# Optimization experiments

Hardware: AMD Instinct MI355X
Metric: run time of the kernel (lower is better)

## Reference

```python
import jax, jax.numpy as jnp
import numpy as np
import math

B, N_TOK, C, H = 8, 1024, 384, 6
K, S, P = 3, 2, 1
OUT_C, HID = 384, 4 * 384
EPS = 1e-5
NEG_INF = float('-inf')


def _build_conv_mask(num_token, k, s, p):
    """Replicates ConvAttentionMask (include_cls_token=True). Returns (mask[(N+2),(N+2)], idx[(W,k^2)] with -1 for padding)."""
    I = int(math.sqrt(num_token))
    ref = np.arange(num_token).reshape(I, I)
    ref = np.pad(ref, ((0, p), (0, p)), constant_values=-1)
    cent = np.arange(k // 2 - p, I - k // 2 + p, s)
    cc = np.stack(np.meshgrid(cent, cent, indexing='ij'), -1).reshape(-1, 1, 2)  # cartesian_prod order
    ke = np.arange(-(k // 2), k // 2 + 1)
    kc = np.stack(np.meshgrid(ke, ke, indexing='ij'), -1).reshape(1, -1, 2)
    coords = cc + kc  # (W, k^2, 2); negative coords wrap like torch fancy indexing -> hit -1 padding
    idx = ref[coords[..., 0], coords[..., 1]]  # (W, k^2)
    mask = np.full((num_token, num_token), NEG_INF, np.float32)
    for w in idx:
        v = w[w >= 0]
        mask[np.ix_(v, v)] = 1.0
    idx = idx + (idx >= 0).astype(np.int32)  # shift for cls token; -1 stays -1
    mask = np.pad(mask, ((1, 0), (1, 0)), constant_values=1.0)  # cls row/col
    mask = np.pad(mask, ((0, 1), (0, 1)), constant_values=0.0)  # extra zero-padded token
    return mask, idx

MASK_NP, IDX_NP = _build_conv_mask(N_TOK, K, S, P)
W_WIN = IDX_NP.shape[0]
# torch negative index -1 on a length-(N_TOK+1) tensor -> wrap to last token
IDX_FLAT = np.where(IDX_NP < 0, IDX_NP + N_TOK + 1, IDX_NP).reshape(-1)


def _ln(x, w, b):
    mu = jnp.mean(x, -1, keepdims=True)
    var = jnp.mean(jnp.square(x - mu), -1, keepdims=True)
    return (x - mu) * jax.lax.rsqrt(var + EPS) * w + b


def setup_inputs() -> dict:
    key = jax.random.key(0)
    ks = jax.random.split(key, 8)
    sd = 0.02
    return {
        'x': jax.random.normal(ks[0], (B, N_TOK + 1, C), jnp.float32),
        'norm1_w': jnp.ones((C,), jnp.float32), 'norm1_b': jnp.zeros((C,), jnp.float32),
        'qkv_w': sd * jax.random.normal(ks[1], (3 * C, C), jnp.float32),
        'proj_w': sd * jax.random.normal(ks[2], (C, C), jnp.float32),
        'proj_b': jnp.zeros((C,), jnp.float32),
        'norm2_w': jnp.ones((C,), jnp.float32), 'norm2_b': jnp.zeros((C,), jnp.float32),
        'pool_w': sd * jax.random.normal(ks[3], (C, K * K * C), jnp.float32),
        'pool_b': jnp.zeros((C,), jnp.float32),
        'norm3_w': jnp.ones((C,), jnp.float32), 'norm3_b': jnp.zeros((C,), jnp.float32),
        'fc1_w': sd * jax.random.normal(ks[4], (HID, C), jnp.float32),
        'fc1_b': jnp.zeros((HID,), jnp.float32),
        'fc2_w': sd * jax.random.normal(ks[5], (OUT_C, HID), jnp.float32),
        'fc2_b': jnp.zeros((OUT_C,), jnp.float32),
    }


def reference(x, norm1_w, norm1_b, qkv_w, proj_w, proj_b, norm2_w, norm2_b,
              pool_w, pool_b, norm3_w, norm3_b, fc1_w, fc1_b, fc2_w, fc2_b):
    mask = jnp.asarray(MASK_NP)  # (N_TOK+2, N_TOK+2), values in {-inf, 0, 1}
    Bv, N, Cv = x.shape
    d = Cv // H
    h = _ln(x, norm1_w, norm1_b)
    h = jnp.pad(h, ((0, 0), (0, 1), (0, 0)))  # append zero token -> (B, N+1, C)
    M = N + 1
    # attention (scale = num_heads**-0.5 as in the source, qkv has no bias)
    qkv = (h @ qkv_w.T).reshape(Bv, M, 3, H, d).transpose(2, 0, 3, 1, 4)
    q, k, v = qkv[0], qkv[1], qkv[2]
    scores = jnp.einsum('bhqd,bhkd->bhqk', q, k) * (H ** -0.5)
    # multiplicative mask {-inf,0,1}: keep where 1, zero where 0, -inf where -inf (intended semantics)
    scores = jnp.where(mask == 1.0, scores, jnp.where(mask == 0.0, 0.0, NEG_INF))
    probs = jax.nn.softmax(scores, axis=-1)
    attn = jnp.einsum('bhqk,bhkd->bhqd', probs, v).transpose(0, 2, 1, 3).reshape(Bv, M, Cv)
    attn = attn @ proj_w.T + proj_b
    h = h + attn
    h = h[:, :-1, :]  # drop padded token -> (B, N, C)
    h = _ln(h, norm2_w, norm2_b)
    # conv-style pooling: gather k^2 tokens per window, project
    gathered = h[:, IDX_FLAT, :].reshape(Bv, W_WIN, K * K * Cv)
    tok = gathered @ pool_w.T + pool_b  # (B, W, C)
    h = jnp.concatenate([h[:, :1, :], tok], axis=1)  # prepend cls -> (B, W+1, C)
    h = _ln(h, norm3_w, norm3_b)
    h = jax.nn.gelu(h @ fc1_w.T + fc1_b, approximate=False)
    return h @ fc2_w.T + fc2_b  # (B, W+1, OUT_C)
```

## Files before the change

kernel.cpp:

```cpp
#include <hip/hip_runtime.h>


typedef unsigned short u16;
typedef unsigned int u32;
typedef short s16x8 __attribute__((ext_vector_type(8)));
typedef float f32x4 __attribute__((ext_vector_type(4)));

__device__ __forceinline__ float b2f(u16 u) {
    return __uint_as_float(((u32)u) << 16);
}
__device__ __forceinline__ u16 f2b(float f) {
    u32 u = __float_as_uint(f);
    return (u16)((u + 0x7FFFu + ((u >> 16) & 1u)) >> 16);
}
__device__ __forceinline__ void gload16(const void* g, void* l) {
    __builtin_amdgcn_global_load_lds(
        (const __attribute__((address_space(1))) void*)g,
        (__attribute__((address_space(3))) void*)l, 16, 0, 0);
}
__device__ __forceinline__ float wave_sum(float v) {
#pragma unroll
    for (int o = 32; o > 0; o >>= 1) v += __shfl_xor(v, o, 64);
    return v;
}
__device__ __forceinline__ float wave_max(float v) {
#pragma unroll
    for (int o = 32; o > 0; o >>= 1) v = fmaxf(v, __shfl_xor(v, o, 64));
    return v;
}
__device__ __forceinline__ float half_sum(float v) {
#pragma unroll
    for (int o = 16; o > 0; o >>= 1) v += __shfl_xor(v, o, 64);
    return v;
}
__device__ __forceinline__ float half_max(float v) {
#pragma unroll
    for (int o = 16; o > 0; o >>= 1) v = fmaxf(v, __shfl_xor(v, o, 64));
    return v;
}
__device__ __forceinline__ float dot8(const float* qsh, int d0, uint4 u) {
    return qsh[d0 + 0] * b2f((u16)(u.x)) + qsh[d0 + 1] * b2f((u16)(u.x >> 16)) +
           qsh[d0 + 2] * b2f((u16)(u.y)) + qsh[d0 + 3] * b2f((u16)(u.y >> 16)) +
           qsh[d0 + 4] * b2f((u16)(u.z)) + qsh[d0 + 5] * b2f((u16)(u.z >> 16)) +
           qsh[d0 + 6] * b2f((u16)(u.w)) + qsh[d0 + 7] * b2f((u16)(u.w >> 16));
}

#define CCH 384
#define SCALE 0.40824829046386302f
#define NEG_BIG (-1e30f)

#define W_QKV 0
#define W_PROJ 442368
#define W_POOL 589824
#define W_FC1 1916928
#define W_FC2 2506752
#define W_TOTAL 3096576

__device__ __forceinline__ void ln_from_f32(const float* in, const float* w,
                                            const float* bb, u16* out,
                                            int lane) {
    float v[6];
    float s = 0.f, ss = 0.f;
#pragma unroll
    for (int i = 0; i < 6; i++) {
        v[i] = in[lane + 64 * i];
        s += v[i];
        ss += v[i] * v[i];
    }
    s = wave_sum(s);
    ss = wave_sum(ss);
    float mu = s * (1.f / 384.f);
    float var = ss * (1.f / 384.f) - mu * mu;
    float inv = rsqrtf(var + 1e-5f);
#pragma unroll
    for (int i = 0; i < 6; i++) {
        int c = lane + 64 * i;
        out[c] = f2b((v[i] - mu) * inv * w[c] + bb[c]);
    }
}
__device__ __forceinline__ void ln_from_b16(const u16* in, const float* w,
                                            const float* bb, u16* out,
                                            int lane) {
    float v[6];
    float s = 0.f, ss = 0.f;
#pragma unroll
    for (int i = 0; i < 6; i++) {
        v[i] = b2f(in[lane + 64 * i]);
        s += v[i];
        ss += v[i] * v[i];
    }
    s = wave_sum(s);
    ss = wave_sum(ss);
    float mu = s * (1.f / 384.f);
    float var = ss * (1.f / 384.f) - mu * mu;
    float inv = rsqrtf(var + 1e-5f);
#pragma unroll
    for (int i = 0; i < 6; i++) {
        int c = lane + 64 * i;
        out[c] = f2b((v[i] - mu) * inv * w[c] + bb[c]);
    }
}

#define PRO_LN 2052
#define PRO_CVT 1512
#define PRO_ZERO 771
__global__ __launch_bounds__(256) void prologue(
    const float* __restrict__ x, const float* __restrict__ n1w,
    const float* __restrict__ n1b, u16* __restrict__ h1,
    const float* __restrict__ qkv_w, const float* __restrict__ proj_w,
    const float* __restrict__ pool_w, const float* __restrict__ fc1_w,
    const float* __restrict__ fc2_w, u16* __restrict__ wb,
    float* __restrict__ dout) {
    int bid = blockIdx.x, tid = threadIdx.x;
    if (bid < PRO_LN) {
        int wv = tid >> 6, lane = tid & 63;
        int row = bid * 4 + wv;
        int t = row % 1026, b = row / 1026;
        u16* out = h1 + (size_t)row * CCH;
        if (t == 1025) {
#pragma unroll
            for (int i = 0; i < 6; i++) out[lane + 64 * i] = 0;
            return;
        }
        ln_from_f32(x + ((size_t)b * 1025 + t) * CCH, n1w, n1b, out, lane);
    } else if (bid < PRO_LN + PRO_CVT) {
        size_t off = ((size_t)(bid - PRO_LN) * 256 + tid) * 8;
        if (off >= W_TOTAL) return;
        const float* src;
        size_t base;
        if (off < W_PROJ)       { src = qkv_w;  base = W_QKV; }
        else if (off < W_POOL)  { src = proj_w; base = W_PROJ; }
        else if (off < W_FC1)   { src = pool_w; base = W_POOL; }
        else if (off < W_FC2)   { src = fc1_w;  base = W_FC1; }
        else                    { src = fc2_w;  base = W_FC2; }
        size_t rel = off - base;
        float4 a = *(const float4*)(src + rel);
        float4 b = *(const float4*)(src + rel + 4);
        uint4 o;
        o.x = (u32)f2b(a.x) | ((u32)f2b(a.y) << 16);
        o.y = (u32)f2b(a.z) | ((u32)f2b(a.w) << 16);
        o.z = (u32)f2b(b.x) | ((u32)f2b(b.y) << 16);
        o.w = (u32)f2b(b.z) | ((u32)f2b(b.w) << 16);
        *(uint4*)(wb + off) = o;
    } else {
        size_t idx = ((size_t)(bid - PRO_LN - PRO_CVT) * 256 + tid) * 4;
        *(float4*)(dout + idx) = make_float4(0.f, 0.f, 0.f, 0.f);
    }
}

#define MID_LN 2050
#define MID_ZERO 768
__global__ __launch_bounds__(256) void midk(u16* __restrict__ h,
                                            const float* __restrict__ n2w,
                                            const float* __restrict__ n2b,
                                            float* __restrict__ tokf) {
    int bid = blockIdx.x, tid = threadIdx.x;
    if (bid < MID_LN) {
        int wv = tid >> 6, lane = tid & 63;
        int row = bid * 4 + wv;
        int b = row / 1025, t = row % 1025;
        u16* p = h + ((size_t)b * 1026 + t) * CCH;
        ln_from_b16(p, n2w, n2b, p, lane);
    } else {
        size_t idx = ((size_t)(bid - MID_LN) * 256 + tid) * 4;
        *(float4*)(tokf + idx) = make_float4(0.f, 0.f, 0.f, 0.f);
    }
}

__global__ __launch_bounds__(256) void ln3_concat(const u16* __restrict__ h2,
                                                  const float* __restrict__ tokf,
                                                  const float* __restrict__ w,
                                                  const float* __restrict__ bb,
                                                  u16* __restrict__ h3) {
    int tid = threadIdx.x;
    int wv = tid >> 6, lane = tid & 63;
    int row = blockIdx.x * 4 + wv;
    int b = row / 257, t = row % 257;
    u16* out = h3 + (size_t)row * CCH;
    if (t == 0) {
        ln_from_b16(h2 + (size_t)b * 1026 * CCH, w, bb, out, lane);
    } else {
        ln_from_f32(tokf + ((size_t)b * 256 + (t - 1)) * CCH, w, bb, out, lane);
    }
}

template <int TN, bool GATHER, int SPLITK, bool BIAS, bool GELU_ACT, bool RES,
          bool ATOMIC>
__global__ __launch_bounds__(256) void gemm_mf(const u16* __restrict__ A,
                                               int lda,
                                               const u16* __restrict__ Bwb,
                                               const float* __restrict__ bias,
                                               const u16* __restrict__ Res,
                                               void* __restrict__ Yv, int M,
                                               int N, int K) {
    __shared__ u16 Asl[128 * 32];
    __shared__ u16 Bsl[TN * 32];
    const int tid = threadIdx.x;
    const int wave = tid >> 6, lane = tid & 63;
    const int quad = lane >> 4, l15 = lane & 15;
    const int wvu = __builtin_amdgcn_readfirstlane(wave);
    const int m0 = blockIdx.y * 128, n0 = blockIdx.x * TN;
    const int kp = (SPLITK > 1) ? blockIdx.z : 0;
    const int KS = K / SPLITK;
    const int kbase = kp * KS;
    const int srow = tid >> 2;
    const int sseg = (tid & 3) ^ (srow & 3);

    f32x4 acc[2][TN / 16];
#pragma unroll
    for (int i = 0; i < 2; i++)
#pragma unroll
        for (int j = 0; j < TN / 16; j++) acc[i][j] = (f32x4){0.f, 0.f, 0.f, 0.f};

    for (int kt = 0; kt < KS; kt += 32) {
        const int kk = kbase + kt;
        const int kf = kk + sseg * 8;
#pragma unroll
        for (int L = 0; L < 2; L++) {
            int row = L * 64 + srow;
            const u16* src;
            if (GATHER) {
                int m = m0 + row;
                int b = m >> 8, w = m & 255;
                int j = kf / 384, rem = kf - j * 384;
                int pr = 2 * (w >> 4) + j / 3 - 1;
                int pc = 2 * (w & 15) + j % 3 - 1;
                int tok = (pr >= 0 && pr < 32 && pc >= 0 && pc < 32)
                              ? (32 * pr + pc + 1)
                              : 1024;
                src = A + ((size_t)b * 1026 + tok) * 384 + rem;
            } else {
                int m = m0 + row;
                if (m >= M) m = M - 1;
                src = A + (size_t)m * lda + kf;
            }
            gload16(src, &Asl[(size_t)(L * 256 + wvu * 64) * 8]);
        }
#pragma unroll
        for (int L = 0; L < TN / 64; L++) {
            int row = L * 64 + srow;
            gload16(Bwb + (size_t)(n0 + row) * K + kf,
                    &Bsl[(size_t)(L * 256 + wvu * 64) * 8]);
        }
        __syncthreads();
        s16x8 afr[2], bfr[TN / 16];
        const int rslot = (quad ^ (l15 & 3)) * 8;
#pragma unroll
        for (int ms = 0; ms < 2; ms++)
            afr[ms] =
                *(const s16x8*)(&Asl[(wave * 32 + ms * 16 + l15) * 32 + rslot]);
#pragma unroll
        for (int ns = 0; ns < TN / 16; ns++)
            bfr[ns] = *(const s16x8*)(&Bsl[(ns * 16 + l15) * 32 + rslot]);
#pragma unroll
        for (int ms = 0; ms < 2; ms++)
#pragma unroll
            for (int ns = 0; ns < TN / 16; ns++)
                acc[ms][ns] = __builtin_amdgcn_mfma_f32_16x16x32_bf16(
                    afr[ms], bfr[ns], acc[ms][ns], 0, 0, 0);
        __syncthreads();
    }
#pragma unroll
    for (int ms = 0; ms < 2; ms++) {
#pragma unroll
        for (int ns = 0; ns < TN / 16; ns++) {
            int n = n0 + ns * 16 + l15;
#pragma unroll
            for (int i = 0; i < 4; i++) {
                int m = m0 + wave * 32 + ms * 16 + quad * 4 + i;
                if (m >= M) continue;
                float v = acc[ms][ns][i];
                if (BIAS && (SPLITK == 1 || kp == 0)) v += bias[n];
                if (RES) v += b2f(Res[(size_t)m * N + n]);
                if (GELU_ACT) v = 0.5f * v * (1.f + erff(v * 0.70710678118f));
                if (ATOMIC)
                    atomicAdd((float*)Yv + (size_t)m * N + n, v);
                else
                    ((u16*)Yv)[(size_t)m * N + n] = f2b(v);
            }
        }
    }
}

__global__ __launch_bounds__(1024) void attn_win(u16* __restrict__ qkv) {
    int bid = blockIdx.x;
    int tid = threadIdx.x;
    if (bid < 48) {
        int h = bid % 6, b = bid / 6;
        u16* base = qkv + (size_t)b * 1026 * 1152 + h * 64;
        int lane = tid & 63, wv = tid >> 6;
        __shared__ float sc[1026];
        __shared__ float qsh[64];
        __shared__ float redmax[16], redsum[16];
        __shared__ float pv[16][64];
        if (tid < 64) qsh[tid] = b2f(base[tid]);
        __syncthreads();
        for (int key = tid; key < 1026; key += 1024) {
            const u16* krow = base + (size_t)key * 1152 + 384;
            float acc = 0.f;
#pragma unroll
            for (int d0 = 0; d0 < 64; d0 += 8)
                acc += dot8(qsh, d0, *(const uint4*)(krow + d0));
            sc[key] = acc * SCALE;
        }
        __syncthreads();
        float lm = NEG_BIG;
        for (int key = tid; key < 1026; key += 1024) lm = fmaxf(lm, sc[key]);
        lm = wave_max(lm);
        if (lane == 0) redmax[wv] = lm;
        __syncthreads();
        float mx = NEG_BIG;
#pragma unroll
        for (int i = 0; i < 16; i++) mx = fmaxf(mx, redmax[i]);
        float lsum = 0.f;
        for (int key = tid; key < 1026; key += 1024) {
            float e = expf(sc[key] - mx);
            sc[key] = e;
            lsum += e;
        }
        lsum = wave_sum(lsum);
        if (lane == 0) redsum[wv] = lsum;
        __syncthreads();
        float Z = 0.f;
#pragma unroll
        for (int i = 0; i < 16; i++) Z += redsum[i];
        float acc = 0.f;
#pragma unroll
        for (int t = 0; t < 65; t++) {
            int key = wv + 16 * t;
            bool ok = key < 1026;
            int kc = ok ? key : 1025;
            float p = ok ? sc[kc] : 0.f;
            acc += p * b2f(base[(size_t)kc * 1152 + 768 + lane]);
        }
        pv[wv][lane] = acc;
        __syncthreads();
        if (tid < 64) {
            float s = 0.f;
#pragma unroll
            for (int w2 = 0; w2 < 16; w2++) s += pv[w2][tid];
            base[tid] = f2b(s / Z);
            base[(size_t)1025 * 1152 + tid] = 0;
        }
        return;
    }
    __shared__ float qshp[16][2][64];
    int wv = tid >> 6, lane = tid & 63;
    int pair = (bid - 48) * 16 + wv;
    int idx = pair & 511;
    int hb = pair >> 9;
    int h = hb % 6, b = hb / 6;
    int hl = lane >> 5, l5 = lane & 31;
    int p0 = idx * 2;
    int p = p0 | hl;
    int r = p >> 5, c = p & 31;
    int rlo, rhi, clo, chi;
    if (r & 1) { rlo = (r - 2 < 0) ? 0 : r - 2; rhi = (r + 2 > 31) ? 31 : r + 2; }
    else       { rlo = (r - 1 < 0) ? 0 : r - 1; rhi = (r + 1 > 31) ? 31 : r + 1; }
    if (c & 1) { clo = (c - 2 < 0) ? 0 : c - 2; chi = (c + 2 > 31) ? 31 : c + 2; }
    else       { clo = (c - 1 < 0) ? 0 : c - 1; chi = (c + 1 > 31) ? 31 : c + 1; }
    int nr = rhi - rlo + 1, nc = chi - clo + 1;
    int nk = nr * nc + 1;
    int tok = 0;
    if (l5 >= 1 && l5 < nk) {
        int jj = l5 - 1;
        tok = 1 + ((rlo + jj / nc) << 5) + (clo + jj % nc);
    }
    u16* base = qkv + (size_t)b * 1026 * 1152 + h * 64;
    qshp[wv][0][lane] = b2f(base[(size_t)(1 + p0) * 1152 + lane]);
    qshp[wv][1][lane] = b2f(base[(size_t)(2 + p0) * 1152 + lane]);
    float sc = NEG_BIG;
    if (l5 < nk) {
        const u16* krow = base + (size_t)tok * 1152 + 384;
        float acc = 0.f;
#pragma unroll
        for (int d0 = 0; d0 < 64; d0 += 8)
            acc += dot8(qshp[wv][hl], d0, *(const uint4*)(krow + d0));
        sc = acc * SCALE;
    }
    float mx = fmaxf(half_max(sc), 0.f);
    float pe = (l5 < nk) ? expf(sc - mx) : 0.f;
    float Z = half_sum(pe) + expf(-mx);
    float o0 = 0.f, o1 = 0.f;
#pragma unroll
    for (int j = 0; j < 26; j++) {
        int t = __shfl(tok, (hl << 5) | j, 64);
        float wj = __shfl(pe, (hl << 5) | j, 64);
        u32 vv = *(const u32*)(base + (size_t)t * 1152 + 768 + 2 * l5);
        o0 += wj * b2f((u16)vv);
        o1 += wj * b2f((u16)(vv >> 16));
    }
    float zi = 1.f / Z;
    u32 packed = (u32)f2b(o0 * zi) | ((u32)f2b(o1 * zi) << 16);
    *(u32*)(base + (size_t)(1 + p) * 1152 + 2 * l5) = packed;
}

extern "C" void kernel_launch(void* const* d_in, const int* in_sizes, int n_in,
                              void* d_out, int out_size, void* d_ws,
                              size_t ws_size, hipStream_t stream) {
    const float* x      = (const float*)d_in[0];
    const float* n1w    = (const float*)d_in[1];
    const float* n1b    = (const float*)d_in[2];
    const float* qkv_w  = (const float*)d_in[3];
    const float* proj_w = (const float*)d_in[4];
    const float* proj_b = (const float*)d_in[5];
    const float* n2w    = (const float*)d_in[6];
    const float* n2b    = (const float*)d_in[7];
    const float* pool_w = (const float*)d_in[8];
    const float* pool_b = (const float*)d_in[9];
    const float* n3w    = (const float*)d_in[10];
    const float* n3b    = (const float*)d_in[11];
    const float* fc1_w  = (const float*)d_in[12];
    const float* fc1_b  = (const float*)d_in[13];
    const float* fc2_w  = (const float*)d_in[14];
    const float* fc2_b  = (const float*)d_in[15];

    u16* ws = (u16*)d_ws;
    u16* h1    = ws;
    u16* qkvb  = ws + 3151872;
    u16* wb    = ws + 12607488;
    float* tokf = (float*)qkvb;
    u16* h3    = qkvb + 1572864;
    u16* mlp1  = qkvb + 2362368;

    prologue<<<PRO_LN + PRO_CVT + PRO_ZERO, 256, 0, stream>>>(
        x, n1w, n1b, h1, qkv_w, proj_w, pool_w, fc1_w, fc2_w, wb,
        (float*)d_out);
    gemm_mf<128, false, 1, false, false, false, false>
        <<<dim3(1152 / 128, 65), 256, 0, stream>>>(h1, 384, wb + W_QKV,
                                                   nullptr, nullptr, qkvb,
                                                   8208, 1152, 384);
    attn_win<<<48 + 24576 / 16, 1024, 0, stream>>>(qkvb);
    gemm_mf<64, false, 1, true, false, true, false>
        <<<dim3(384 / 64, 65), 256, 0, stream>>>(qkvb, 1152, wb + W_PROJ,
                                                 proj_b, h1, h1, 8208, 384,
                                                 384);
    midk<<<MID_LN + MID_ZERO, 256, 0, stream>>>(h1, n2w, n2b, tokf);
    gemm_mf<64, true, 4, true, false, false, true>
        <<<dim3(384 / 64, 16, 4), 256, 0, stream>>>(h1, 384, wb + W_POOL,
                                                    pool_b, nullptr, tokf,
                                                    2048, 384, 3456);
    ln3_concat<<<8 * 257 / 4, 256, 0, stream>>>(h1, tokf, n3w, n3b, h3);
    gemm_mf<64, false, 1, true, true, false, false>
        <<<dim3(1536 / 64, 17), 256, 0, stream>>>(h3, 384, wb + W_FC1, fc1_b,
                                                  nullptr, mlp1, 2056, 1536,
                                                  384);
    gemm_mf<64, false, 4, true, false, false, true>
        <<<dim3(384 / 64, 17, 4), 256, 0, stream>>>(mlp1, 1536, wb + W_FC2,
                                                    fc2_b, nullptr, d_out,
                                                    2056, 384, 1536);
}
```

Baseline: 257.8 us.

## Double-buffer LDS tiles in MFMA GEMM to overlap global loads with compute

```diff
diff --git a/kernel.cpp b/kernel.cpp
--- a/kernel.cpp
+++ b/kernel.cpp
@@ -193,8 +193,8 @@
                                                const u16* __restrict__ Res,
                                                void* __restrict__ Yv, int M,
                                                int N, int K) {
-    __shared__ u16 Asl[128 * 32];
-    __shared__ u16 Bsl[TN * 32];
+    __shared__ u16 Asl[2][128 * 32];
+    __shared__ u16 Bsl[2][TN * 32];
     const int tid = threadIdx.x;
     const int wave = tid >> 6, lane = tid & 63;
     const int quad = lane >> 4, l15 = lane & 15;
@@ -212,8 +212,7 @@
 #pragma unroll
         for (int j = 0; j < TN / 16; j++) acc[i][j] = (f32x4){0.f, 0.f, 0.f, 0.f};
 
-    for (int kt = 0; kt < KS; kt += 32) {
-        const int kk = kbase + kt;
+    auto stage = [&](int buf, int kk) {
         const int kf = kk + sseg * 8;
 #pragma unroll
         for (int L = 0; L < 2; L++) {
@@ -234,31 +233,50 @@
                 if (m >= M) m = M - 1;
                 src = A + (size_t)m * lda + kf;
             }
-            gload16(src, &Asl[(size_t)(L * 256 + wvu * 64) * 8]);
+            gload16(src, &Asl[buf][(size_t)(L * 256 + wvu * 64) * 8]);
         }
 #pragma unroll
         for (int L = 0; L < TN / 64; L++) {
             int row = L * 64 + srow;
             gload16(Bwb + (size_t)(n0 + row) * K + kf,
-                    &Bsl[(size_t)(L * 256 + wvu * 64) * 8]);
-        }
-        __syncthreads();
+                    &Bsl[buf][(size_t)(L * 256 + wvu * 64) * 8]);
+        }
+    };
+
+    int cur = 0;
+    stage(0, kbase);
+    for (int kt = 0; kt < KS; kt += 32) {
+        const bool more = (kt + 32 < KS);
+        if (more) {
+            stage(cur ^ 1, kbase + kt + 32);
+            if (TN == 64)
+                asm volatile("s_waitcnt vmcnt(3)" ::: "memory");
+            else
+                asm volatile("s_waitcnt vmcnt(4)" ::: "memory");
+        } else {
+            asm volatile("s_waitcnt vmcnt(0)" ::: "memory");
+        }
+        __builtin_amdgcn_s_barrier();
+        __builtin_amdgcn_sched_barrier(0);
         s16x8 afr[2], bfr[TN / 16];
         const int rslot = (quad ^ (l15 & 3)) * 8;
 #pragma unroll
         for (int ms = 0; ms < 2; ms++)
-            afr[ms] =
-                *(const s16x8*)(&Asl[(wave * 32 + ms * 16 + l15) * 32 + rslot]);
+            afr[ms] = *(const s16x8*)(&Asl[cur][(wave * 32 + ms * 16 + l15) * 32 +
+                                               rslot]);
 #pragma unroll
         for (int ns = 0; ns < TN / 16; ns++)
-            bfr[ns] = *(const s16x8*)(&Bsl[(ns * 16 + l15) * 32 + rslot]);
+            bfr[ns] = *(const s16x8*)(&Bsl[cur][(ns * 16 + l15) * 32 + rslot]);
 #pragma unroll
         for (int ms = 0; ms < 2; ms++)
 #pragma unroll
             for (int ns = 0; ns < TN / 16; ns++)
                 acc[ms][ns] = __builtin_amdgcn_mfma_f32_16x16x32_bf16(
                     afr[ms], bfr[ns], acc[ms][ns], 0, 0, 0);
-        __syncthreads();
+        asm volatile("s_waitcnt lgkmcnt(0)" ::: "memory");
+        __builtin_amdgcn_sched_barrier(0);
+        __builtin_amdgcn_s_barrier();
+        cur ^= 1;
     }
 #pragma unroll
     for (int ms = 0; ms < 2; ms++) {
```

Result: no change. 261.0 us (+1.2%).
